# Kernel optimization log

Hardware: AMD Instinct MI355X
Metric: run time of the kernel (lower is better)

Reference implementation:

```python
import jax, jax.numpy as jnp
from jax import lax
import numpy as np

B, T, C, HID, H, W = 8, 24, 3, 32, 64, 64


def setup_inputs() -> dict:
    key = jax.random.key(0)
    ks = jax.random.split(key, 8)
    def n(k, shape, s=0.05):
        return jax.random.normal(k, shape, dtype=jnp.float32) * s
    return {
        "x": n(ks[0], (B, T, C, H, W), 1.0),
        # encoder layer 0: conv over concat(x, h) -> 4*HID gate channels
        "Wenc0": n(ks[1], (4 * HID, C + HID, 3, 3)),
        "benc0": jnp.zeros((4 * HID,), jnp.float32),
        # encoder layer 1: input is layer-0 hidden seq (HID channels)
        "Wenc1": n(ks[2], (4 * HID, HID + HID, 3, 3)),
        "benc1": jnp.zeros((4 * HID,), jnp.float32),
        # decoder (1 layer, input_dim channels in)
        "Wdec": n(ks[3], (4 * HID, C + HID, 3, 3)),
        "bdec": jnp.zeros((4 * HID,), jnp.float32),
        # MLP head: HID*H*W -> 256 -> 97
        "fc1_w": n(ks[4], (256, HID * H * W), 0.01),
        "fc1_b": jnp.zeros((256,), jnp.float32),
        "fc2_w": n(ks[5], (97, 256)),
        "fc2_b": jnp.zeros((97,), jnp.float32),
    }


def _cell_step(h, c, x_t, Wk, b):
    # ConvLSTM cell: conv(concat(x,h)) -> i,f,o,g gates
    z = lax.conv_general_dilated(
        jnp.concatenate([x_t, h], axis=1), Wk,
        window_strides=(1, 1), padding='SAME',
        dimension_numbers=('NCHW', 'OIHW', 'NCHW')) + b[None, :, None, None]
    i, f, o, g = jnp.split(z, 4, axis=1)
    c_new = jax.nn.sigmoid(f) * c + jax.nn.sigmoid(i) * jnp.tanh(g)
    h_new = jax.nn.sigmoid(o) * jnp.tanh(c_new)
    return h_new, c_new


def _run_layer(x_tb, Wk, b):
    # x_tb: [T, B, Cin, H, W]; zero-initialized state
    h0 = jnp.zeros((x_tb.shape[1], HID, H, W), x_tb.dtype)
    c0 = jnp.zeros_like(h0)
    def step(hc, xt):
        h, c = _cell_step(hc[0], hc[1], xt, Wk, b)
        return (h, c), h
    (hT, cT), hs = lax.scan(step, (h0, c0), x_tb)
    return hs, (hT, cT)


def reference(x, Wenc0, benc0, Wenc1, benc1, Wdec, bdec, fc1_w, fc1_b, fc2_w, fc2_b):
    x_tb = jnp.transpose(x, (1, 0, 2, 3, 4))          # [T,B,C,H,W]
    hs0, _ = _run_layer(x_tb, Wenc0, benc0)           # layer-0 hidden seq
    _, (hT, cT) = _run_layer(hs0, Wenc1, benc1)       # last-layer final state
    # decoder: one step on last input frame, seeded with encoder state
    h_dec, _ = _cell_step(hT, cT, x[:, -1], Wdec, bdec)  # [B,HID,H,W]
    feat = h_dec.reshape(h_dec.shape[0], -1)          # [B, HID*H*W]
    hdn = jax.nn.relu(feat @ fc1_w.T + fc1_b)
    return hdn @ fc2_w.T + fc2_b                      # [B, 97]
```

## Files before the change

kernel.cpp:

```cpp
#include <hip/hip_runtime.h>

typedef __attribute__((ext_vector_type(8))) short short8v;
typedef __attribute__((ext_vector_type(4))) float f32x4;
typedef __attribute__((ext_vector_type(4))) unsigned int uint4v;
typedef unsigned short u16;

__device__ __forceinline__ u16 f2bf(float f) {
  unsigned u = __float_as_uint(f);
  u += 0x7FFFu + ((u >> 16) & 1u);
  return (u16)(u >> 16);
}
__device__ __forceinline__ short8v ld8(const u16* p) {
  return *reinterpret_cast<const short8v*>(p);
}
__device__ __forceinline__ float frcp(float x) { return __builtin_amdgcn_rcpf(x); }

__device__ __forceinline__ void st_cg(u16* p, uint4v v) {
  asm volatile("global_store_dwordx4 %0, %1, off sc0 sc1" :: "v"(p), "v"(v) : "memory");
}
__device__ __forceinline__ void ld2_cg(const u16* a0, const u16* a1,
                                       uint4v& v0, uint4v& v1) {
  asm volatile(
      "global_load_dwordx4 %0, %2, off sc0 sc1\n\t"
      "global_load_dwordx4 %1, %3, off sc0 sc1\n\t"
      "s_waitcnt vmcnt(0)"
      : "=&v"(v0), "=&v"(v1) : "v"(a0), "v"(a1) : "memory");
}

__device__ __forceinline__ void poll_lane(const unsigned* a, unsigned tgt, bool active) {
  bool pending = active;
  while (__ballot(pending)) {
    if (pending &&
        __hip_atomic_load((unsigned*)a, __ATOMIC_RELAXED, __HIP_MEMORY_SCOPE_AGENT) >= tgt)
      pending = false;
    if (__ballot(pending)) __builtin_amdgcn_s_sleep(1);
  }
}
__device__ __forceinline__ void publish(unsigned* f, unsigned v) {
  __syncthreads();
  if (threadIdx.x == 0)
    __hip_atomic_store(f, v, __ATOMIC_RELAXED, __HIP_MEMORY_SCOPE_AGENT);
}

__global__ void k_pack(const float* __restrict__ We0, const float* __restrict__ We1,
                       const float* __restrict__ Wd,
                       u16* __restrict__ Wh0p, u16* __restrict__ Wx1p,
                       u16* __restrict__ Wh1p, u16* __restrict__ Whdp,
                       u16* __restrict__ Wx0p, u16* __restrict__ Wxdp,
                       unsigned* __restrict__ flags) {
  int i = blockIdx.x * 256 + threadIdx.x;
  if (i < 8192) flags[i] = 0u;
  if (i < 147456) {
    int tbl = i / 36864, j = i % 36864;
    int s = j >> 12, cg = (j >> 11) & 1, gate = (j >> 9) & 3,
        chl = (j >> 5) & 15, ci = j & 31;
    int co = gate * 32 + cg * 16 + chl;
    float v;
    if (tbl == 0)      v = We0[(co * 35 + 3 + ci) * 9 + s];
    else if (tbl == 1) v = We1[(co * 64 + ci) * 9 + s];
    else if (tbl == 2) v = We1[(co * 64 + 32 + ci) * 9 + s];
    else               v = Wd[(co * 35 + 3 + ci) * 9 + s];
    u16* dst = tbl == 0 ? Wh0p : tbl == 1 ? Wx1p : tbl == 2 ? Wh1p : Whdp;
    dst[j] = f2bf(v);
  } else {
    int j = i - 147456, tbl = j >> 12;
    j &= 4095;
    int cg = (j >> 11) & 1, gate = (j >> 9) & 3, chl = (j >> 5) & 15, k = j & 31;
    int co = gate * 32 + cg * 16 + chl;
    const float* src = tbl ? Wd : We0;
    u16 v = (k < 27) ? f2bf(src[(co * 35 + (k % 3)) * 9 + (k / 3)]) : (u16)0;
    (tbl ? Wxdp : Wx0p)[j] = v;
  }
}

__global__ void k_im2col(const float* __restrict__ x, u16* __restrict__ out) {
  int p = blockIdx.x * 256 + threadIdx.x;
  int t = p >> 15;
  int rem = p & 32767;
  int b = rem >> 12;
  int yy = (rem >> 6) & 63;
  int xx = rem & 63;
  __align__(16) u16 buf[32];
#pragma unroll
  for (int k = 27; k < 32; k++) buf[k] = 0;
  const float* xb = x + ((size_t)(b * 24 + t)) * 3 * 4096;
#pragma unroll
  for (int ky = 0; ky < 3; ky++) {
    int ys = yy + ky - 1;
    bool yok = (unsigned)ys < 64u;
#pragma unroll
    for (int kx = 0; kx < 3; kx++) {
      int xs = xx + kx - 1;
      bool ok = yok && ((unsigned)xs < 64u);
#pragma unroll
      for (int ci = 0; ci < 3; ci++) {
        float v = ok ? xb[(size_t)ci * 4096 + ys * 64 + xs] : 0.f;
        buf[(ky * 3 + kx) * 3 + ci] = f2bf(v);
      }
    }
  }
  uint4v* dst = (uint4v*)(out + (size_t)p * 32);
  const uint4v* s = (const uint4v*)buf;
  dst[0] = s[0]; dst[1] = s[1]; dst[2] = s[2]; dst[3] = s[3];
}

__global__ __launch_bounds__(512, 1) void k_persist(
    const u16* __restrict__ imc, u16* __restrict__ hs0G, u16* __restrict__ h1G,
    const u16* __restrict__ Wx0, const u16* __restrict__ Wh0,
    const float* __restrict__ be0,
    const u16* __restrict__ Wx1, const u16* __restrict__ Wh1,
    const float* __restrict__ be1,
    const u16* __restrict__ Wxd, const u16* __restrict__ Whd,
    const float* __restrict__ bd,
    float* __restrict__ hdec, unsigned* __restrict__ flag) {
  __shared__ __align__(16) u16 smH0[8448];
  __shared__ __align__(16) u16 smH1[8448];
  const int bid = blockIdx.x;
  const int b = bid & 7;
  const int yblk = bid >> 3;
  const int y0 = yblk << 1;
  const int fi = bid * 16;
  const int tid = threadIdx.x;
  const int w = tid >> 6, l = tid & 63, lr = l & 15, g = l >> 4;
  const bool isL1w = w >= 4;
  const int lw = w & 3, mh = lw >> 1, cg = lw & 1, y = y0 + mh;
  const int ch = cg * 16 + lr;

  if (tid < 64) {
    int q = tid & 31;
    int rgq = q >> 1, side = q & 1;
    u16* base = (tid < 32 ? smH0 : smH1) + ((size_t)(rgq * 66 + side * 65)) * 8;
    *(uint4v*)base = (uint4v)0u;
  }

  const float* bia = isL1w ? be1 : be0;
  const float bI = bia[ch], bF = bia[32 + ch], bO = bia[64 + ch], bG = bia[96 + ch];
  float cr[16];
#pragma unroll
  for (int i = 0; i < 16; i++) cr[i] = 0.f;

  const int sthr = tid & 255;
  const int sgrp = tid >> 8;
  const int pxs = sthr >> 2, gqs = sthr & 3;
  const size_t rbG = (size_t)b * 131072;
  const size_t poff = (size_t)pxs * 32 + gqs * 8;
  const int rup = (yblk == 0) ? y0 : y0 - 1;
  const int rdn = (yblk == 31) ? y0 + 1 : y0 + 2;
  u16* smS = sgrp ? smH1 : smH0;
  u16* dUp = smS + ((size_t)(gqs * 66 + pxs + 1)) * 8;
  u16* dDn = smS + ((size_t)((12 + gqs) * 66 + pxs + 1)) * 8;

  auto do_shifts = [&](const u16* sm, const u16* __restrict__ W, f32x4 (&acc)[4][4]) {
#pragma unroll
    for (int sft = 0; sft < 9; sft++) {
      const int ky = sft / 3, dx = sft % 3 - 1;
      const u16* wb = W + ((size_t)(sft * 2 + cg) * 64 + lr) * 32 + g * 8;
      short8v B0 = ld8(wb), B1 = ld8(wb + 512), B2 = ld8(wb + 1024), B3 = ld8(wb + 1536);
      const u16* abase = sm + ((size_t)(((mh + ky) * 4 + g) * 66 + lr + dx + 1)) * 8;
#pragma unroll
      for (int mt = 0; mt < 4; mt++) {
        short8v A = ld8(abase + mt * 128);
        acc[mt][0] = __builtin_amdgcn_mfma_f32_16x16x32_bf16(A, B0, acc[mt][0], 0, 0, 0);
        acc[mt][1] = __builtin_amdgcn_mfma_f32_16x16x32_bf16(A, B1, acc[mt][1], 0, 0, 0);
        acc[mt][2] = __builtin_amdgcn_mfma_f32_16x16x32_bf16(A, B2, acc[mt][2], 0, 0, 0);
        acc[mt][3] = __builtin_amdgcn_mfma_f32_16x16x32_bf16(A, B3, acc[mt][3], 0, 0, 0);
      }
    }
  };
  auto imcol = [&](const u16* xp, const u16* __restrict__ W, f32x4 (&acc)[4][4]) {
    const u16* ab = xp + rbG + (size_t)y * 2048 + g * 8;
    const u16* wb = W + (cg * 64 + lr) * 32 + g * 8;
    short8v B0 = ld8(wb), B1 = ld8(wb + 512), B2 = ld8(wb + 1024), B3 = ld8(wb + 1536);
#pragma unroll
    for (int mt = 0; mt < 4; mt++) {
      short8v A = ld8(ab + (mt * 16 + lr) * 32);
      acc[mt][0] = __builtin_amdgcn_mfma_f32_16x16x32_bf16(A, B0, acc[mt][0], 0, 0, 0);
      acc[mt][1] = __builtin_amdgcn_mfma_f32_16x16x32_bf16(A, B1, acc[mt][1], 0, 0, 0);
      acc[mt][2] = __builtin_amdgcn_mfma_f32_16x16x32_bf16(A, B2, acc[mt][2], 0, 0, 0);
      acc[mt][3] = __builtin_amdgcn_mfma_f32_16x16x32_bf16(A, B3, acc[mt][3], 0, 0, 0);
    }
  };
  auto gates = [&](f32x4 (&acc)[4][4], u16* hbf) {
#pragma unroll
    for (int mt = 0; mt < 4; mt++) {
#pragma unroll
      for (int j = 0; j < 4; j++) {
        float zi = acc[mt][0][j] + bI, zf = acc[mt][1][j] + bF;
        float zo = acc[mt][2][j] + bO, zg = acc[mt][3][j] + bG;
        float ei = __expf(-zi), ef = __expf(-zf), eo = __expf(-zo);
        float eg = __expf(2.f * zg);
        float cn = frcp(1.f + ef) * cr[mt * 4 + j] +
                   (eg - 1.f) * frcp((1.f + ei) * (eg + 1.f));
        float ec = __expf(2.f * cn);
        cr[mt * 4 + j] = cn;
        hbf[mt * 4 + j] = f2bf((ec - 1.f) * frcp((1.f + eo) * (ec + 1.f)));
      }
    }
  };

  for (int s = 0; s <= 25; ++s) {
    if (s > 0 && tid < 64) {
      const unsigned* a = nullptr; bool act = false;
      if (l == 0 && yblk > 0)  { a = flag + fi - 128; act = true; }
      if (l == 1 && yblk < 31) { a = flag + fi + 128; act = true; }
      poll_lane(a, (unsigned)s, act);
    }
    __syncthreads();

    if (sgrp == 0 && s >= 1 && s <= 24) {
      const u16* src = hs0G + (size_t)((s - 1) & 1) * 1048576 + rbG;
      uint4v v0, v1;
      ld2_cg(src + (size_t)rup * 2048 + poff, src + (size_t)rdn * 2048 + poff, v0, v1);
      if (yblk == 0)  v0 = (uint4v)0u;
      if (yblk == 31) v1 = (uint4v)0u;
      *(uint4v*)dUp = v0; *(uint4v*)dDn = v1;
    }
    if (sgrp == 1 && s >= 2) {
      const u16* src = h1G + (size_t)(s & 1) * 1048576 + rbG;
      uint4v v0, v1;
      ld2_cg(src + (size_t)rup * 2048 + poff, src + (size_t)rdn * 2048 + poff, v0, v1);
      if (yblk == 0)  v0 = (uint4v)0u;
      if (yblk == 31) v1 = (uint4v)0u;
      *(uint4v*)dUp = v0; *(uint4v*)dDn = v1;
    }
    __syncthreads();

    if (s == 25) {
      if (isL1w) {
        f32x4 acc[4][4];
#pragma unroll
        for (int i = 0; i < 4; i++)
#pragma unroll
          for (int j = 0; j < 4; j++) acc[i][j] = (f32x4)0.f;
        imcol(imc + (size_t)23 * 1048576, Wxd, acc);
        do_shifts(smH1, Whd, acc);
        const float bId = bd[ch], bFd = bd[32 + ch], bOd = bd[64 + ch], bGd = bd[96 + ch];
#pragma unroll
        for (int mt = 0; mt < 4; mt++) {
#pragma unroll
          for (int j = 0; j < 4; j++) {
            int px = mt * 16 + g * 4 + j;
            float zi = acc[mt][0][j] + bId, zf = acc[mt][1][j] + bFd;
            float zo = acc[mt][2][j] + bOd, zg = acc[mt][3][j] + bGd;
            float ei = __expf(-zi), ef = __expf(-zf), eo = __expf(-zo);
            float eg = __expf(2.f * zg);
            float cn = frcp(1.f + ef) * cr[mt * 4 + j] +
                       (eg - 1.f) * frcp((1.f + ei) * (eg + 1.f));
            float ec = __expf(2.f * cn);
            float hn = (ec - 1.f) * frcp((1.f + eo) * (ec + 1.f));
            hdec[((size_t)(b * 32 + ch) * 64 + y) * 64 + px] = hn;
          }
        }
      }
      return;
    }

    const bool doL0 = !isL1w && s <= 23;
    const bool doL1 = isL1w && s >= 1 && s <= 24;
    u16 hbf[16];

    if (doL0) {
      f32x4 acc[4][4];
#pragma unroll
      for (int i = 0; i < 4; i++)
#pragma unroll
        for (int j = 0; j < 4; j++) acc[i][j] = (f32x4)0.f;
      imcol(imc + (size_t)s * 1048576, Wx0, acc);
      if (s >= 1) do_shifts(smH0, Wh0, acc);
      gates(acc, hbf);
    }
    if (doL1) {
      f32x4 acc[4][4];
#pragma unroll
      for (int i = 0; i < 4; i++)
#pragma unroll
        for (int j = 0; j < 4; j++) acc[i][j] = (f32x4)0.f;
      do_shifts(smH0, Wx1, acc);
      if (s >= 2) do_shifts(smH1, Wh1, acc);
      gates(acc, hbf);
    }
    __syncthreads();

    if (doL0 || doL1) {
      u16* smD = isL1w ? smH1 : smH0;
#pragma unroll
      for (int mt = 0; mt < 4; mt++)
#pragma unroll
        for (int j = 0; j < 4; j++) {
          int px = mt * 16 + g * 4 + j;
          smD[((size_t)((1 + mh) * 4 + (ch >> 3)) * 66 + px + 1) * 8 + (ch & 7)] =
              hbf[mt * 4 + j];
        }
    }
    __syncthreads();

    if (sgrp == 0 && s <= 23) {
      u16* d = hs0G + (size_t)(s & 1) * 1048576 + rbG;
      st_cg(d + (size_t)y0 * 2048 + poff,
            *(const uint4v*)(smH0 + ((size_t)(4 + gqs) * 66 + pxs + 1) * 8));
      st_cg(d + (size_t)(y0 + 1) * 2048 + poff,
            *(const uint4v*)(smH0 + ((size_t)(8 + gqs) * 66 + pxs + 1) * 8));
    }
    if (sgrp == 1 && s >= 1 && s <= 24) {
      u16* d = h1G + (size_t)((s - 1) & 1) * 1048576 + rbG;
      st_cg(d + (size_t)y0 * 2048 + poff,
            *(const uint4v*)(smH1 + ((size_t)(4 + gqs) * 66 + pxs + 1) * 8));
      st_cg(d + (size_t)(y0 + 1) * 2048 + poff,
            *(const uint4v*)(smH1 + ((size_t)(8 + gqs) * 66 + pxs + 1) * 8));
    }
    publish(flag + fi, (unsigned)(s + 1));
  }
}

__global__ __launch_bounds__(256) void k_fc1(const float* __restrict__ w,
                                             const float* __restrict__ feat,
                                             float* __restrict__ partial) {
  __shared__ float fsm[8][1024];
  const int ng = blockIdx.x, ks = blockIdx.y;
  const int tid = threadIdx.x;
  const float* fb = feat + (size_t)ks * 1024;
  for (int i = tid; i < 2048; i += 256) {
    int bb = i >> 8, kk = (i & 255) << 2;
    *(f32x4*)&fsm[bb][kk] = *(const f32x4*)(fb + (size_t)bb * 131072 + kk);
  }
  __syncthreads();
  const int wv = tid >> 6, lane = tid & 63;
  const int n0 = ng * 16 + wv * 4;
  const float* wr = w + (size_t)n0 * 131072 + (size_t)ks * 1024;
  float acc[4][8];
#pragma unroll
  for (int i = 0; i < 4; i++)
#pragma unroll
    for (int j = 0; j < 8; j++) acc[i][j] = 0.f;
#pragma unroll
  for (int it = 0; it < 4; it++) {
    int k = it * 256 + lane * 4;
    f32x4 w0 = *(const f32x4*)(wr + k);
    f32x4 w1 = *(const f32x4*)(wr + 131072 + k);
    f32x4 w2 = *(const f32x4*)(wr + 262144 + k);
    f32x4 w3 = *(const f32x4*)(wr + 393216 + k);
#pragma unroll
    for (int bb = 0; bb < 8; bb++) {
      f32x4 fv = *(const f32x4*)&fsm[bb][k];
      acc[0][bb] += w0[0] * fv[0] + w0[1] * fv[1] + w0[2] * fv[2] + w0[3] * fv[3];
      acc[1][bb] += w1[0] * fv[0] + w1[1] * fv[1] + w1[2] * fv[2] + w1[3] * fv[3];
      acc[2][bb] += w2[0] * fv[0] + w2[1] * fv[1] + w2[2] * fv[2] + w2[3] * fv[3];
      acc[3][bb] += w3[0] * fv[0] + w3[1] * fv[1] + w3[2] * fv[2] + w3[3] * fv[3];
    }
  }
#pragma unroll
  for (int nn = 0; nn < 4; nn++)
#pragma unroll
    for (int bb = 0; bb < 8; bb++) {
      float v = acc[nn][bb];
#pragma unroll
      for (int m = 32; m >= 1; m >>= 1) v += __shfl_xor(v, m, 64);
      if (lane == 0) partial[((size_t)ks * 8 + bb) * 256 + n0 + nn] = v;
    }
}

__global__ void k_fc1_fin(const float* __restrict__ partial,
                          const float* __restrict__ b1, float* __restrict__ hdn) {
  int i = blockIdx.x * 256 + threadIdx.x;
  if (i >= 2048) return;
  int b = i >> 8, n = i & 255;
  float v = b1[n];
  for (int ks = 0; ks < 128; ks++) v += partial[((size_t)ks * 8 + b) * 256 + n];
  hdn[i] = fmaxf(v, 0.f);
}

__global__ void k_fc2(const float* __restrict__ hdn, const float* __restrict__ w2,
                      const float* __restrict__ b2, float* __restrict__ out) {
  int i = blockIdx.x * 256 + threadIdx.x;
  if (i >= 776) return;
  int b = i / 97, m = i % 97;
  const float* h = hdn + b * 256;
  const float* wr = w2 + m * 256;
  float v = b2[m];
  for (int k = 0; k < 256; k++) v += h[k] * wr[k];
  out[i] = v;
}

extern "C" void kernel_launch(void* const* d_in, const int* in_sizes, int n_in,
                              void* d_out, int out_size, void* d_ws, size_t ws_size,
                              hipStream_t stream) {
  const float* x   = (const float*)d_in[0];
  const float* We0 = (const float*)d_in[1];
  const float* be0 = (const float*)d_in[2];
  const float* We1 = (const float*)d_in[3];
  const float* be1 = (const float*)d_in[4];
  const float* Wd  = (const float*)d_in[5];
  const float* bd  = (const float*)d_in[6];
  const float* f1w = (const float*)d_in[7];
  const float* f1b = (const float*)d_in[8];
  const float* f2w = (const float*)d_in[9];
  const float* f2b = (const float*)d_in[10];

  char* ws = (char*)d_ws;
  u16*      imc  = (u16*)(ws + 0);
  u16*      hs0G = (u16*)(ws + 50331648);
  u16*      h1G  = (u16*)(ws + 54525952);
  u16*      wp   = (u16*)(ws + 58720256);
  float*    hdec = (float*)(ws + 62914560);
  unsigned* flag = (unsigned*)(ws + 67108864);
  float*    part = (float*)(ws + 0);
  float*    hdn  = (float*)(ws + 1048576);
  u16 *Wh0p = wp, *Wx1p = wp + 36864, *Wh1p = wp + 73728, *Whdp = wp + 110592,
      *Wx0p = wp + 147456, *Wxdp = wp + 151552;

  k_pack<<<608, 256, 0, stream>>>(We0, We1, Wd, Wh0p, Wx1p, Wh1p, Whdp, Wx0p,
                                  Wxdp, flag);
  k_im2col<<<3072, 256, 0, stream>>>(x, imc);

  k_persist<<<256, 512, 0, stream>>>(imc, hs0G, h1G, Wx0p, Wh0p, be0,
                                     Wx1p, Wh1p, be1, Wxdp, Whdp, bd, hdec, flag);

  k_fc1<<<dim3(16, 128), 256, 0, stream>>>(f1w, hdec, part);
  k_fc1_fin<<<8, 256, 0, stream>>>(part, f1b, hdn);
  k_fc2<<<4, 256, 0, stream>>>(hdn, f2w, f2b, (float*)d_out);
}
```

Measured before the change: 337.1 us.

## Overlap halo-row loads with interior conv MFMAs via async global-to-LDS loads

Replaces the blocking register-staged halo row loads with asynchronous global_load_lds transfers issued directly into shared memory. Each step's conv is split so the kernel rows that do not touch the halo row are computed while the halo load is in flight. Only after a vmcnt wait and barrier are the halo-dependent kernel row's MFMAs done. This hides the cross-block neighbor-row load latency behind compute in the serial recurrence, at the cost of splitting the accumulation into two passes and holding the accumulators across the barrier.

```diff
diff --git a/kernel.cpp b/kernel.cpp
--- a/kernel.cpp
+++ b/kernel.cpp
@@ -18,13 +18,13 @@
 __device__ __forceinline__ void st_cg(u16* p, uint4v v) {
   asm volatile("global_store_dwordx4 %0, %1, off sc0 sc1" :: "v"(p), "v"(v) : "memory");
 }
-__device__ __forceinline__ void ld2_cg(const u16* a0, const u16* a1,
-                                       uint4v& v0, uint4v& v1) {
-  asm volatile(
-      "global_load_dwordx4 %0, %2, off sc0 sc1\n\t"
-      "global_load_dwordx4 %1, %3, off sc0 sc1\n\t"
-      "s_waitcnt vmcnt(0)"
-      : "=&v"(v0), "=&v"(v1) : "v"(a0), "v"(a1) : "memory");
+__device__ __forceinline__ void gload16(const u16* g, u16* l) {
+  __builtin_amdgcn_global_load_lds(
+      (const __attribute__((address_space(1))) void*)g,
+      (__attribute__((address_space(3))) void*)l, 16, 0, 0x11);
+}
+__device__ __forceinline__ void wait_vm0() {
+  asm volatile("s_waitcnt vmcnt(0)" ::: "memory");
 }
 
 __device__ __forceinline__ void poll_lane(const unsigned* a, unsigned tgt, bool active) {
@@ -125,6 +125,7 @@
   const bool isL1w = w >= 4;
   const int lw = w & 3, mh = lw >> 1, cg = lw & 1, y = y0 + mh;
   const int ch = cg * 16 + lr;
+  const int kyHalo = mh ? 2 : 0;
 
   if (tid < 64) {
     int q = tid & 31;
@@ -139,21 +140,26 @@
 #pragma unroll
   for (int i = 0; i < 16; i++) cr[i] = 0.f;
 
+  const int sw = w & 3;
+  const int sg = w >> 2;
+  u16* smS = sg ? smH1 : smH0;
+  u16* ldsUp = smS + ((size_t)(sw * 66 + 1)) * 8;
+  u16* ldsDn = smS + ((size_t)((12 + sw) * 66 + 1)) * 8;
+  const size_t rbG = (size_t)b * 131072;
+  const size_t lsrc = (size_t)l * 32 + sw * 8;
+
   const int sthr = tid & 255;
   const int sgrp = tid >> 8;
   const int pxs = sthr >> 2, gqs = sthr & 3;
-  const size_t rbG = (size_t)b * 131072;
   const size_t poff = (size_t)pxs * 32 + gqs * 8;
-  const int rup = (yblk == 0) ? y0 : y0 - 1;
-  const int rdn = (yblk == 31) ? y0 + 1 : y0 + 2;
-  u16* smS = sgrp ? smH1 : smH0;
-  u16* dUp = smS + ((size_t)(gqs * 66 + pxs + 1)) * 8;
-  u16* dDn = smS + ((size_t)((12 + gqs) * 66 + pxs + 1)) * 8;
-
-  auto do_shifts = [&](const u16* sm, const u16* __restrict__ W, f32x4 (&acc)[4][4]) {
+
+  auto do_shifts = [&](const u16* sm, const u16* __restrict__ W, f32x4 (&acc)[4][4],
+                       int kyOnly, int kySkip) {
 #pragma unroll
     for (int sft = 0; sft < 9; sft++) {
       const int ky = sft / 3, dx = sft % 3 - 1;
+      if (kyOnly >= 0 && ky != kyOnly) continue;
+      if (kySkip >= 0 && ky == kySkip) continue;
       const u16* wb = W + ((size_t)(sft * 2 + cg) * 64 + lr) * 32 + g * 8;
       short8v B0 = ld8(wb), B1 = ld8(wb + 512), B2 = ld8(wb + 1024), B3 = ld8(wb + 1536);
       const u16* abase = sm + ((size_t)(((mh + ky) * 4 + g) * 66 + lr + dx + 1)) * 8;
@@ -207,41 +213,57 @@
     }
     __syncthreads();
 
-    if (sgrp == 0 && s >= 1 && s <= 24) {
-      const u16* src = hs0G + (size_t)((s - 1) & 1) * 1048576 + rbG;
-      uint4v v0, v1;
-      ld2_cg(src + (size_t)rup * 2048 + poff, src + (size_t)rdn * 2048 + poff, v0, v1);
-      if (yblk == 0)  v0 = (uint4v)0u;
-      if (yblk == 31) v1 = (uint4v)0u;
-      *(uint4v*)dUp = v0; *(uint4v*)dDn = v1;
-    }
-    if (sgrp == 1 && s >= 2) {
-      const u16* src = h1G + (size_t)(s & 1) * 1048576 + rbG;
-      uint4v v0, v1;
-      ld2_cg(src + (size_t)rup * 2048 + poff, src + (size_t)rdn * 2048 + poff, v0, v1);
-      if (yblk == 0)  v0 = (uint4v)0u;
-      if (yblk == 31) v1 = (uint4v)0u;
-      *(uint4v*)dUp = v0; *(uint4v*)dDn = v1;
-    }
+    const bool stg = sg ? (s >= 2) : (s >= 1 && s <= 24);
+    if (stg) {
+      const u16* src = sg ? (h1G + (size_t)(s & 1) * 1048576 + rbG)
+                          : (hs0G + (size_t)((s - 1) & 1) * 1048576 + rbG);
+      if (yblk > 0)
+        gload16(src + (size_t)(y0 - 1) * 2048 + lsrc, ldsUp);
+      else
+        *(uint4v*)(ldsUp + (size_t)l * 8) = (uint4v)0u;
+      if (yblk < 31)
+        gload16(src + (size_t)(y0 + 2) * 2048 + lsrc, ldsDn);
+      else
+        *(uint4v*)(ldsDn + (size_t)l * 8) = (uint4v)0u;
+    }
+
+    const bool doL0 = !isL1w && s <= 23;
+    const bool doL1 = isL1w && s >= 1 && s <= 24;
+    f32x4 acc[4][4];
+#pragma unroll
+    for (int i = 0; i < 4; i++)
+#pragma unroll
+      for (int j = 0; j < 4; j++) acc[i][j] = (f32x4)0.f;
+
+    if (doL0) {
+      imcol(imc + (size_t)s * 1048576, Wx0, acc);
+      if (s >= 1) do_shifts(smH0, Wh0, acc, -1, kyHalo);
+    }
+    if (doL1) {
+      do_shifts(smH0, Wx1, acc, -1, kyHalo);
+      if (s >= 2) do_shifts(smH1, Wh1, acc, -1, kyHalo);
+    }
+
+    wait_vm0();
     __syncthreads();
 
     if (s == 25) {
       if (isL1w) {
-        f32x4 acc[4][4];
+        f32x4 accd[4][4];
 #pragma unroll
         for (int i = 0; i < 4; i++)
 #pragma unroll
-          for (int j = 0; j < 4; j++) acc[i][j] = (f32x4)0.f;
-        imcol(imc + (size_t)23 * 1048576, Wxd, acc);
-        do_shifts(smH1, Whd, acc);
+          for (int j = 0; j < 4; j++) accd[i][j] = (f32x4)0.f;
+        imcol(imc + (size_t)23 * 1048576, Wxd, accd);
+        do_shifts(smH1, Whd, accd, -1, -1);
         const float bId = bd[ch], bFd = bd[32 + ch], bOd = bd[64 + ch], bGd = bd[96 + ch];
 #pragma unroll
         for (int mt = 0; mt < 4; mt++) {
 #pragma unroll
           for (int j = 0; j < 4; j++) {
             int px = mt * 16 + g * 4 + j;
-            float zi = acc[mt][0][j] + bId, zf = acc[mt][1][j] + bFd;
-            float zo = acc[mt][2][j] + bOd, zg = acc[mt][3][j] + bGd;
+            float zi = accd[mt][0][j] + bId, zf = accd[mt][1][j] + bFd;
+            float zo = accd[mt][2][j] + bOd, zg = accd[mt][3][j] + bGd;
             float ei = __expf(-zi), ef = __expf(-zf), eo = __expf(-zo);
             float eg = __expf(2.f * zg);
             float cn = frcp(1.f + ef) * cr[mt * 4 + j] +
@@ -255,28 +277,14 @@
       return;
     }
 
-    const bool doL0 = !isL1w && s <= 23;
-    const bool doL1 = isL1w && s >= 1 && s <= 24;
     u16 hbf[16];
-
     if (doL0) {
-      f32x4 acc[4][4];
-#pragma unroll
-      for (int i = 0; i < 4; i++)
-#pragma unroll
-        for (int j = 0; j < 4; j++) acc[i][j] = (f32x4)0.f;
-      imcol(imc + (size_t)s * 1048576, Wx0, acc);
-      if (s >= 1) do_shifts(smH0, Wh0, acc);
+      if (s >= 1) do_shifts(smH0, Wh0, acc, kyHalo, -1);
       gates(acc, hbf);
     }
     if (doL1) {
-      f32x4 acc[4][4];
-#pragma unroll
-      for (int i = 0; i < 4; i++)
-#pragma unroll
-        for (int j = 0; j < 4; j++) acc[i][j] = (f32x4)0.f;
-      do_shifts(smH0, Wx1, acc);
-      if (s >= 2) do_shifts(smH1, Wh1, acc);
+      do_shifts(smH0, Wx1, acc, kyHalo, -1);
+      if (s >= 2) do_shifts(smH1, Wh1, acc, kyHalo, -1);
       gates(acc, hbf);
     }
     __syncthreads();
```

New measurement: 377.2 us. +11.9%, slower.
